# Kernel tuning notes

Hardware: AMD Instinct MI355X
Metric: run time of the kernel (lower is better)

Reference implementation:

```python
import jax, jax.numpy as jnp
import numpy as np

N = 4096
E = 262144
IN_C = 128
OUT_C = 128
EDGE_D = 16


def setup_inputs() -> dict:
    key = jax.random.key(0)
    k = jax.random.split(key, 8)
    x = jax.random.normal(k[0], (N, IN_C), dtype=jnp.float32)
    edge_index = jax.random.randint(k[1], (2, E), 0, N, dtype=jnp.int64)
    edge_attr = jax.random.normal(k[2], (N, N, EDGE_D), dtype=jnp.float32)
    # nn.Linear params: y = x @ W.T + b; store pre-transposed W for x @ W
    s1 = 1.0 / np.sqrt(IN_C + EDGE_D)
    s2 = 1.0 / np.sqrt(OUT_C)
    W1 = jax.random.uniform(k[3], (IN_C + EDGE_D, OUT_C), jnp.float32, -s1, s1)
    b1 = jax.random.uniform(k[4], (OUT_C,), jnp.float32, -s1, s1)
    W2 = jax.random.uniform(k[5], (OUT_C, OUT_C), jnp.float32, -s2, s2)
    b2 = jax.random.uniform(k[6], (OUT_C,), jnp.float32, -s2, s2)
    return {"x": x, "edge_index": edge_index, "edge_attr": edge_attr,
            "W1": W1, "b1": b1, "W2": W2, "b2": b2}


def reference(x, edge_index, edge_attr, W1, b1, W2, b2):
    row, col = edge_index[0], edge_index[1]
    x_row = x[row]                      # [E, IN_C] gather
    e = edge_attr[row, col]             # [E, EDGE_D] gather from dense NxN table
    h = jnp.concatenate([x_row, e], axis=-1)     # [E, IN_C+EDGE_D]
    h = jax.nn.relu(h @ W1 + b1)                  # [E, OUT_C]
    h = jax.nn.relu(h @ W2 + b2)                  # [E, OUT_C]
    # global_add_pool(out, col): scatter-add edges into node buckets by col
    return jax.ops.segment_sum(h, col, num_segments=x.shape[0])  # [N, OUT_C]
```

## Files before the change

### kernel.cpp

```cpp
#include <hip/hip_runtime.h>
#include <hip/hip_bf16.h>

#define NN 4096
#define IC 128
#define OC 128
#define ED 16
#define EPB 128
#define NT 512
#define NSLOT 8
#define NBLK 256
#define NCPY 8

typedef __bf16 bf16x8 __attribute__((ext_vector_type(8)));
typedef float  f32x16 __attribute__((ext_vector_type(16)));

#define BAR() do { asm volatile("s_waitcnt lgkmcnt(0)" ::: "memory"); \
    __builtin_amdgcn_s_barrier(); \
    __builtin_amdgcn_sched_barrier(0); } while (0)

__device__ __forceinline__ unsigned short bf16u(float f) {
    unsigned int u = __float_as_uint(f);
    u = (u + 0x7FFFu + ((u >> 16) & 1u)) >> 16;
    return (unsigned short)u;
}
__device__ __forceinline__ float bf16tof(unsigned short h) {
    return __uint_as_float(((unsigned int)h) << 16);
}
__device__ __forceinline__ int swzk(int row) { return (row ^ (row >> 3)) & 7; }

__global__ __launch_bounds__(128) void k_xw1(
    const float* __restrict__ x, const float* __restrict__ W1,
    const float* __restrict__ b1, float* __restrict__ xw1b,
    float* __restrict__ out, int* __restrict__ hist8)
{
    __shared__ float xs[8][IC];
    const int t = threadIdx.x;
    const int r0 = blockIdx.x * 8;
    #pragma unroll
    for (int r = 0; r < 8; ++r) xs[r][t] = x[(size_t)(r0 + r) * IC + t];

    const float4 z = make_float4(0.f, 0.f, 0.f, 0.f);
    float4* o4 = (float4*)out;
    o4[blockIdx.x * 256 + t]       = z;
    o4[blockIdx.x * 256 + 128 + t] = z;
    if (blockIdx.x < NCPY) {
        int4* h4 = (int4*)(hist8 + blockIdx.x * 4096);
        #pragma unroll
        for (int j = 0; j < 8; ++j) h4[j * 128 + t] = make_int4(0, 0, 0, 0);
    }

    __syncthreads();
    float acc[8];
    const float bb = b1[t];
    #pragma unroll
    for (int r = 0; r < 8; ++r) acc[r] = bb;
    #pragma unroll 4
    for (int k = 0; k < IC; ++k) {
        const float w = W1[(size_t)k * OC + t];
        #pragma unroll
        for (int r = 0; r < 8; ++r) acc[r] = fmaf(xs[r][k], w, acc[r]);
    }
    #pragma unroll
    for (int r = 0; r < 8; ++r) xw1b[(size_t)(r0 + r) * OC + t] = acc[r];
}

__global__ void k_hist(const int* __restrict__ eidx, int* __restrict__ hist8, int E) {
    const int i = blockIdx.x * blockDim.x + threadIdx.x;
    const int k = blockIdx.x & (NCPY - 1);
    if (i < E) atomicAdd(&hist8[k * 4096 + eidx[E + i]], 1);
}

__global__ __launch_bounds__(256) void k_scan(
    const int* __restrict__ hist8, int* __restrict__ cursor8)
{
    __shared__ int tot[256];
    __shared__ int base[256];
    const int t = threadIdx.x;
    int loc[16];
    int s = 0;
    #pragma unroll
    for (int j = 0; j < 16; ++j) {
        const int b = t * 16 + j;
        int sb = 0;
        #pragma unroll
        for (int k = 0; k < NCPY; ++k) sb += hist8[k * 4096 + b];
        loc[j] = s; s += sb;
    }
    tot[t] = s;
    __syncthreads();
    if (t == 0) {
        int a = 0;
        for (int i = 0; i < 256; ++i) { base[i] = a; a += tot[i]; }
    }
    __syncthreads();
    const int a = base[t];
    #pragma unroll
    for (int j = 0; j < 16; ++j) {
        const int b = t * 16 + j;
        int off = a + loc[j];
        #pragma unroll
        for (int k = 0; k < NCPY; ++k) {
            cursor8[k * 4096 + b] = off;
            off += hist8[k * 4096 + b];
        }
    }
}

__global__ void k_scatter(const int* __restrict__ eidx, int* __restrict__ cursor8,
                          int2* __restrict__ csr, int E) {
    const int i = blockIdx.x * blockDim.x + threadIdx.x;
    const int k = blockIdx.x & (NCPY - 1);
    if (i < E) {
        const int row = eidx[i];
        const int col = eidx[E + i];
        const int pos = atomicAdd(&cursor8[k * 4096 + col], 1);
        csr[pos] = make_int2(row, col);
    }
}

__global__ __launch_bounds__(NT, 2) void k_edge7(
    const int2* __restrict__ csr, const float* __restrict__ eattr,
    const float* __restrict__ xw1b, const float* __restrict__ W1,
    const float* __restrict__ W2, const float* __restrict__ b2,
    float* __restrict__ out, int E)
{
    extern __shared__ char smem[];
    char*   const h1hi = smem;
    char*   const h1lo = smem + 32768;
    float4* const eaL  = (float4*)(smem + 65536);
    float4* const w1L  = (float4*)(smem + 73728);
    float*  const lacc = (float*)(smem + 81920);
    int*    const srowL = (int*)(smem + 86016);
    int*    const scolL = srowL + 256;

    const int t   = threadIdx.x;
    const int l   = t & 63;
    const int wid = t >> 6;
    const int cg  = t & 15, eg = t >> 4;
    const int c0  = cg << 3, e0 = eg << 2;
    const int sz  = (eg >> 1) & 3;
    const int em  = t >> 2, q = t & 3;
    const int esz = (em >> 3) & 3;

    const int ntl = wid & 3;
    const int mh  = wid >> 2;
    const int lm  = l & 31;
    const int hi  = l >> 5;
    const int c2  = ntl * 32 + lm;

    w1L[t] = ((const float4*)(W1 + (size_t)IC * OC))[t];

    bf16x8 w2h[8], w2l[8];
    #pragma unroll
    for (int s = 0; s < 8; ++s) {
        union { unsigned short us[8]; bf16x8 v; } Uh, Ul;
        #pragma unroll
        for (int j = 0; j < 8; ++j) {
            const float w = W2[(size_t)(s * 16 + hi * 8 + j) * OC + c2];
            const unsigned short h = bf16u(w);
            Uh.us[j] = h;
            Ul.us[j] = bf16u(w - bf16tof(h));
        }
        w2h[s] = Uh.v; w2l[s] = Ul.v;
    }
    const float b2s = b2[c2];

    lacc[t] = 0.f; lacc[t + NT] = 0.f;

    const int nper = (E / EPB) / NBLK;
    const int ibb  = blockIdx.x * nper;

    if (t < EPB) {
        const int2 rc = csr[(size_t)ibb * EPB + t];
        srowL[t] = rc.x;
        scolL[t] = rc.y;
    }
    __syncthreads();

    float4 pA;
    {
        const int r = srowL[em], c = scolL[em];
        pA = ((const float4*)(eattr + ((size_t)r * NN + c) * ED))[q];
    }
    int2 pidx;
    {
        const int ibn = (nper > 1) ? 1 : 0;
        pidx = (t < EPB) ? csr[(size_t)(ibb + ibn) * EPB + t] : make_int2(0, 0);
    }

    int cur = 0;
    for (int ii = 0; ii < nper; ++ii) {
        const int nxt = cur ^ 1;

        BAR();

        if (t < EPB) { srowL[nxt * 128 + t] = pidx.x; scolL[nxt * 128 + t] = pidx.y; }
        eaL[(em * 4 + q) ^ esz] = pA;
        float4 xa[4], xb[4];
        #pragma unroll
        for (int ri = 0; ri < 4; ++ri) {
            const int row = srowL[cur * 128 + e0 + ri];
            const float4* p = (const float4*)(xw1b + (size_t)row * OC + c0);
            xa[ri] = p[0]; xb[ri] = p[1];
        }
        BAR();

        float4 ha[4], hb[4];
        #pragma unroll
        for (int ri = 0; ri < 4; ++ri) { ha[ri] = xa[ri]; hb[ri] = xb[ri]; }
        #pragma unroll
        for (int dc = 0; dc < 4; ++dc) {
            float4 ev[4];
            #pragma unroll
            for (int ri = 0; ri < 4; ++ri)
                ev[ri] = eaL[((e0 + ri) * 4 + dc) ^ sz];
            #pragma unroll
            for (int dd = 0; dd < 4; ++dd) {
                const int d = dc * 4 + dd;
                const float4 wA = w1L[d * 32 + cg * 2];
                const float4 wB = w1L[d * 32 + cg * 2 + 1];
                #pragma unroll
                for (int ri = 0; ri < 4; ++ri) {
                    const float evd = (dd == 0) ? ev[ri].x : (dd == 1) ? ev[ri].y
                                     : (dd == 2) ? ev[ri].z : ev[ri].w;
                    ha[ri].x = fmaf(evd, wA.x, ha[ri].x);
                    ha[ri].y = fmaf(evd, wA.y, ha[ri].y);
                    ha[ri].z = fmaf(evd, wA.z, ha[ri].z);
                    ha[ri].w = fmaf(evd, wA.w, ha[ri].w);
                    hb[ri].x = fmaf(evd, wB.x, hb[ri].x);
                    hb[ri].y = fmaf(evd, wB.y, hb[ri].y);
                    hb[ri].z = fmaf(evd, wB.z, hb[ri].z);
                    hb[ri].w = fmaf(evd, wB.w, hb[ri].w);
                }
            }
        }
        #pragma unroll
        for (int ri = 0; ri < 4; ++ri) {
            const int row = e0 + ri;
            float v[8] = { ha[ri].x, ha[ri].y, ha[ri].z, ha[ri].w,
                           hb[ri].x, hb[ri].y, hb[ri].z, hb[ri].w };
            union { unsigned short us[8]; uint4 qv; } Hh, Hl;
            #pragma unroll
            for (int j = 0; j < 8; ++j) {
                const float f = fmaxf(v[j], 0.f);
                const unsigned short h = bf16u(f);
                Hh.us[j] = h;
                Hl.us[j] = bf16u(f - bf16tof(h));
            }
            const int boff = (cg * 16) ^ (swzk(row) << 4);
            *(uint4*)(h1hi + row * 256 + boff) = Hh.qv;
            *(uint4*)(h1lo + row * 256 + boff) = Hl.qv;
        }
        {
            const int r = srowL[nxt * 128 + em], c = scolL[nxt * 128 + em];
            pA = ((const float4*)(eattr + ((size_t)r * NN + c) * ED))[q];
        }
        {
            const int iin = (ii + 2 < nper) ? (ii + 2) : (nper - 1);
            pidx = (t < EPB) ? csr[(size_t)(ibb + iin) * EPB + t] : make_int2(0, 0);
        }
        BAR();

        f32x16 acc0 = (f32x16)(0.0f);
        f32x16 acc1 = (f32x16)(0.0f);
        const int arow0 = (mh * 2 + 0) * 32 + lm;
        const int arow1 = (mh * 2 + 1) * 32 + lm;
        const int ak0 = swzk(arow0) << 4;
        const int ak1 = swzk(arow1) << 4;
        #pragma unroll
        for (int s = 0; s < 8; ++s) {
            const int kb = s * 32 + hi * 16;
            const bf16x8 aH0 = *(const bf16x8*)(h1hi + arow0 * 256 + (kb ^ ak0));
            const bf16x8 aL0 = *(const bf16x8*)(h1lo + arow0 * 256 + (kb ^ ak0));
            const bf16x8 aH1 = *(const bf16x8*)(h1hi + arow1 * 256 + (kb ^ ak1));
            const bf16x8 aL1 = *(const bf16x8*)(h1lo + arow1 * 256 + (kb ^ ak1));
            acc0 = __builtin_amdgcn_mfma_f32_32x32x16_bf16(aH0, w2h[s], acc0, 0, 0, 0);
            acc1 = __builtin_amdgcn_mfma_f32_32x32x16_bf16(aH1, w2h[s], acc1, 0, 0, 0);
            acc0 = __builtin_amdgcn_mfma_f32_32x32x16_bf16(aL0, w2h[s], acc0, 0, 0, 0);
            acc1 = __builtin_amdgcn_mfma_f32_32x32x16_bf16(aL1, w2h[s], acc1, 0, 0, 0);
            acc0 = __builtin_amdgcn_mfma_f32_32x32x16_bf16(aH0, w2l[s], acc0, 0, 0, 0);
            acc1 = __builtin_amdgcn_mfma_f32_32x32x16_bf16(aH1, w2l[s], acc1, 0, 0, 0);
        }

        const int colbase = scolL[cur * 128];
        #pragma unroll
        for (int p = 0; p < 2; ++p) {
            const int mbase = (mh * 2 + p) * 32 + 4 * hi;
            #pragma unroll
            for (int g = 0; g < 4; ++g) {
                const int eb = mbase + 8 * g;
                float sv;
                {
                    const float a0 = (p == 0) ? acc0[4 * g] : acc1[4 * g];
                    sv = fmaxf(a0 + b2s, 0.f);
                }
                int ccur = scolL[cur * 128 + eb];
                #pragma unroll
                for (int j = 1; j < 4; ++j) {
                    const float aj = (p == 0) ? acc0[4 * g + j] : acc1[4 * g + j];
                    const float v = fmaxf(aj + b2s, 0.f);
                    const int c = scolL[cur * 128 + eb + j];
                    if (c == ccur) {
                        sv += v;
                    } else {
                        const int slot = ccur - colbase;
                        if (slot < NSLOT) {
                            if (sv != 0.f) atomicAdd(&lacc[slot * OC + c2], sv);
                        } else {
                            if (sv != 0.f) atomicAdd(&out[(size_t)ccur * OC + c2], sv);
                        }
                        ccur = c; sv = v;
                    }
                }
                const int slot = ccur - colbase;
                if (slot < NSLOT) {
                    if (sv != 0.f) atomicAdd(&lacc[slot * OC + c2], sv);
                } else {
                    if (sv != 0.f) atomicAdd(&out[(size_t)ccur * OC + c2], sv);
                }
            }
        }
        BAR();

        int span = scolL[cur * 128 + 127] - colbase + 1;
        if (span > NSLOT) span = NSLOT;
        for (int idx = t; idx < span * OC; idx += NT) {
            const float v = lacc[idx];
            lacc[idx] = 0.f;
            if (v != 0.f)
                atomicAdd(&out[(size_t)(colbase + (idx >> 7)) * OC + (idx & 127)], v);
        }
        cur = nxt;
    }
}

#define LDS_BYTES 88064

extern "C" void kernel_launch(void* const* d_in, const int* in_sizes, int n_in,
                              void* d_out, int out_size, void* d_ws, size_t ws_size,
                              hipStream_t stream) {
    const float* x    = (const float*)d_in[0];
    const int*   eidx = (const int*)d_in[1];
    const float* ea   = (const float*)d_in[2];
    const float* W1   = (const float*)d_in[3];
    const float* b1   = (const float*)d_in[4];
    const float* W2   = (const float*)d_in[5];
    const float* b2   = (const float*)d_in[6];
    float* out = (float*)d_out;

    const int E = in_sizes[1] / 2;

    char* ws = (char*)d_ws;
    float* xw1b    = (float*)ws;
    int*   hist8   = (int*)(ws + 2097152);
    int*   cursor8 = (int*)(ws + 2097152 + 131072);
    int2*  csr     = (int2*)(ws + 2097152 + 262144);

    k_xw1<<<NN / 8, 128, 0, stream>>>(x, W1, b1, xw1b, out, hist8);
    k_hist<<<(E + 255) / 256, 256, 0, stream>>>(eidx, hist8, E);
    k_scan<<<1, 256, 0, stream>>>(hist8, cursor8);
    k_scatter<<<(E + 255) / 256, 256, 0, stream>>>(eidx, cursor8, csr, E);

    hipFuncSetAttribute(reinterpret_cast<const void*>(k_edge7),
                        hipFuncAttributeMaxDynamicSharedMemorySize, LDS_BYTES);
    k_edge7<<<NBLK, NT, LDS_BYTES, stream>>>(csr, ea, xw1b, W1, W2, b2, out, E);
}
```

Baseline: 138.8 us.

## Halve edge block size to 64 edges and fuse histogram into xw1 kernel

The edge kernel now uses 256-thread blocks that each process 64 edges per tile, with twice as many blocks. This roughly halves LDS per block, which may allow more blocks per CU and finer load balance, and each wave now covers both 32-row M tiles of one output column slice. The separate histogram kernel is removed: histogram counting moves into the xw1 kernel, and hist8 is zeroed by a memset placed before it. This saves one launch, but the extra memset plus the higher per-block overhead from smaller tiles may cost time back.

```diff
diff --git a/kernel.cpp b/kernel.cpp
--- a/kernel.cpp
+++ b/kernel.cpp
@@ -5,10 +5,10 @@
 #define IC 128
 #define OC 128
 #define ED 16
-#define EPB 128
-#define NT 512
+#define EPB 64
+#define NT 256
 #define NSLOT 8
-#define NBLK 256
+#define NBLK 512
 #define NCPY 8
 
 typedef __bf16 bf16x8 __attribute__((ext_vector_type(8)));
@@ -30,8 +30,9 @@
 
 __global__ __launch_bounds__(128) void k_xw1(
     const float* __restrict__ x, const float* __restrict__ W1,
-    const float* __restrict__ b1, float* __restrict__ xw1b,
-    float* __restrict__ out, int* __restrict__ hist8)
+    const float* __restrict__ b1, const int* __restrict__ eidx,
+    float* __restrict__ xw1b, float* __restrict__ out,
+    int* __restrict__ hist8, int E)
 {
     __shared__ float xs[8][IC];
     const int t = threadIdx.x;
@@ -43,10 +44,14 @@
     float4* o4 = (float4*)out;
     o4[blockIdx.x * 256 + t]       = z;
     o4[blockIdx.x * 256 + 128 + t] = z;
-    if (blockIdx.x < NCPY) {
-        int4* h4 = (int4*)(hist8 + blockIdx.x * 4096);
-        #pragma unroll
-        for (int j = 0; j < 8; ++j) h4[j * 128 + t] = make_int4(0, 0, 0, 0);
+
+    {
+        const int e0 = blockIdx.x * 512;
+        #pragma unroll
+        for (int j = 0; j < 4; ++j) {
+            const int k = (2 * blockIdx.x + (j >> 1)) & (NCPY - 1);
+            atomicAdd(&hist8[k * 4096 + eidx[E + e0 + t + j * 128]], 1);
+        }
     }
 
     __syncthreads();
@@ -62,12 +67,6 @@
     }
     #pragma unroll
     for (int r = 0; r < 8; ++r) xw1b[(size_t)(r0 + r) * OC + t] = acc[r];
-}
-
-__global__ void k_hist(const int* __restrict__ eidx, int* __restrict__ hist8, int E) {
-    const int i = blockIdx.x * blockDim.x + threadIdx.x;
-    const int k = blockIdx.x & (NCPY - 1);
-    if (i < E) atomicAdd(&hist8[k * 4096 + eidx[E + i]], 1);
 }
 
 __global__ __launch_bounds__(256) void k_scan(
@@ -118,7 +117,7 @@
     }
 }
 
-__global__ __launch_bounds__(NT, 2) void k_edge7(
+__global__ __launch_bounds__(NT, 2) void k_edge8(
     const int2* __restrict__ csr, const float* __restrict__ eattr,
     const float* __restrict__ xw1b, const float* __restrict__ W1,
     const float* __restrict__ W2, const float* __restrict__ b2,
@@ -126,12 +125,12 @@
 {
     extern __shared__ char smem[];
     char*   const h1hi = smem;
-    char*   const h1lo = smem + 32768;
-    float4* const eaL  = (float4*)(smem + 65536);
-    float4* const w1L  = (float4*)(smem + 73728);
-    float*  const lacc = (float*)(smem + 81920);
-    int*    const srowL = (int*)(smem + 86016);
-    int*    const scolL = srowL + 256;
+    char*   const h1lo = smem + 16384;
+    float4* const eaL  = (float4*)(smem + 32768);
+    float4* const w1L  = (float4*)(smem + 36864);
+    float*  const lacc = (float*)(smem + 45056);
+    int*    const srowL = (int*)(smem + 49152);
+    int*    const scolL = srowL + 128;
 
     const int t   = threadIdx.x;
     const int l   = t & 63;
@@ -142,13 +141,12 @@
     const int em  = t >> 2, q = t & 3;
     const int esz = (em >> 3) & 3;
 
-    const int ntl = wid & 3;
-    const int mh  = wid >> 2;
     const int lm  = l & 31;
     const int hi  = l >> 5;
-    const int c2  = ntl * 32 + lm;
-
-    w1L[t] = ((const float4*)(W1 + (size_t)IC * OC))[t];
+    const int c2  = wid * 32 + lm;
+
+    w1L[t]       = ((const float4*)(W1 + (size_t)IC * OC))[t];
+    w1L[t + NT]  = ((const float4*)(W1 + (size_t)IC * OC))[t + NT];
 
     bf16x8 w2h[8], w2l[8];
     #pragma unroll
@@ -165,7 +163,8 @@
     }
     const float b2s = b2[c2];
 
-    lacc[t] = 0.f; lacc[t + NT] = 0.f;
+    #pragma unroll
+    for (int i = 0; i < 4; ++i) lacc[t + NT * i] = 0.f;
 
     const int nper = (E / EPB) / NBLK;
     const int ibb  = blockIdx.x * nper;
@@ -194,12 +193,12 @@
 
         BAR();
 
-        if (t < EPB) { srowL[nxt * 128 + t] = pidx.x; scolL[nxt * 128 + t] = pidx.y; }
+        if (t < EPB) { srowL[nxt * EPB + t] = pidx.x; scolL[nxt * EPB + t] = pidx.y; }
         eaL[(em * 4 + q) ^ esz] = pA;
         float4 xa[4], xb[4];
         #pragma unroll
         for (int ri = 0; ri < 4; ++ri) {
-            const int row = srowL[cur * 128 + e0 + ri];
+            const int row = srowL[cur * EPB + e0 + ri];
             const float4* p = (const float4*)(xw1b + (size_t)row * OC + c0);
             xa[ri] = p[0]; xb[ri] = p[1];
         }
@@ -252,7 +251,7 @@
             *(uint4*)(h1lo + row * 256 + boff) = Hl.qv;
         }
         {
-            const int r = srowL[nxt * 128 + em], c = scolL[nxt * 128 + em];
+            const int r = srowL[nxt * EPB + em], c = scolL[nxt * EPB + em];
             pA = ((const float4*)(eattr + ((size_t)r * NN + c) * ED))[q];
         }
         {
@@ -263,8 +262,8 @@
 
         f32x16 acc0 = (f32x16)(0.0f);
         f32x16 acc1 = (f32x16)(0.0f);
-        const int arow0 = (mh * 2 + 0) * 32 + lm;
-        const int arow1 = (mh * 2 + 1) * 32 + lm;
+        const int arow0 = lm;
+        const int arow1 = 32 + lm;
         const int ak0 = swzk(arow0) << 4;
         const int ak1 = swzk(arow1) << 4;
         #pragma unroll
@@ -282,10 +281,10 @@
             acc1 = __builtin_amdgcn_mfma_f32_32x32x16_bf16(aH1, w2l[s], acc1, 0, 0, 0);
         }
 
-        const int colbase = scolL[cur * 128];
+        const int colbase = scolL[cur * EPB];
         #pragma unroll
         for (int p = 0; p < 2; ++p) {
-            const int mbase = (mh * 2 + p) * 32 + 4 * hi;
+            const int mbase = p * 32 + 4 * hi;
             #pragma unroll
             for (int g = 0; g < 4; ++g) {
                 const int eb = mbase + 8 * g;
@@ -294,12 +293,12 @@
                     const float a0 = (p == 0) ? acc0[4 * g] : acc1[4 * g];
                     sv = fmaxf(a0 + b2s, 0.f);
                 }
-                int ccur = scolL[cur * 128 + eb];
+                int ccur = scolL[cur * EPB + eb];
                 #pragma unroll
                 for (int j = 1; j < 4; ++j) {
                     const float aj = (p == 0) ? acc0[4 * g + j] : acc1[4 * g + j];
                     const float v = fmaxf(aj + b2s, 0.f);
-                    const int c = scolL[cur * 128 + eb + j];
+                    const int c = scolL[cur * EPB + eb + j];
                     if (c == ccur) {
                         sv += v;
                     } else {
@@ -322,7 +321,7 @@
         }
         BAR();
 
-        int span = scolL[cur * 128 + 127] - colbase + 1;
+        int span = scolL[cur * EPB + EPB - 1] - colbase + 1;
         if (span > NSLOT) span = NSLOT;
         for (int idx = t; idx < span * OC; idx += NT) {
             const float v = lacc[idx];
@@ -334,7 +333,7 @@
     }
 }
 
-#define LDS_BYTES 88064
+#define LDS_BYTES 50176
 
 extern "C" void kernel_launch(void* const* d_in, const int* in_sizes, int n_in,
                               void* d_out, int out_size, void* d_ws, size_t ws_size,
@@ -356,12 +355,12 @@
     int*   cursor8 = (int*)(ws + 2097152 + 131072);
     int2*  csr     = (int2*)(ws + 2097152 + 262144);
 
-    k_xw1<<<NN / 8, 128, 0, stream>>>(x, W1, b1, xw1b, out, hist8);
-    k_hist<<<(E + 255) / 256, 256, 0, stream>>>(eidx, hist8, E);
+    hipMemsetAsync(hist8, 0, 131072, stream);
+    k_xw1<<<NN / 8, 128, 0, stream>>>(x, W1, b1, eidx, xw1b, out, hist8, E);
     k_scan<<<1, 256, 0, stream>>>(hist8, cursor8);
     k_scatter<<<(E + 255) / 256, 256, 0, stream>>>(eidx, cursor8, csr, E);
 
-    hipFuncSetAttribute(reinterpret_cast<const void*>(k_edge7),
+    hipFuncSetAttribute(reinterpret_cast<const void*>(k_edge8),
                         hipFuncAttributeMaxDynamicSharedMemorySize, LDS_BYTES);
-    k_edge7<<<NBLK, NT, LDS_BYTES, stream>>>(csr, ea, xw1b, W1, W2, b2, out, E);
-}
+    k_edge8<<<NBLK, NT, LDS_BYTES, stream>>>(csr, ea, xw1b, W1, W2, b2, out, E);
+}
```

Measured after the change: 140.9 us. About the same (+1.5%).
